# Kernel tuning notes

Hardware: AMD Instinct MI355X
Metric: run time of the kernel (lower is better)

## Reference

```python
import jax, jax.numpy as jnp
import numpy as np

B, T, F, H = 512, 512, 32, 64  # batch, lag, n_features, hidden_sizes[0]


def _lstm_layer(x_seq, Wih, Whh, bih, bhh):
    """Single LSTM layer, batch_first input [B,T,Fin] -> [B,T,H].
    PyTorch gate order: i, f, g, o."""
    # Precompute input projections for all timesteps (one big GEMM)
    xg = jnp.einsum('btf,gf->btg', x_seq, Wih) + bih + bhh  # [B,T,4H]
    xg_t = jnp.transpose(xg, (1, 0, 2))  # [T,B,4H]
    h0 = jnp.zeros((x_seq.shape[0], Whh.shape[1]), x_seq.dtype)
    c0 = jnp.zeros_like(h0)

    def step(carry, g_t):
        h, c = carry
        gates = g_t + h @ Whh.T  # [B,4H]
        i, f, g, o = jnp.split(gates, 4, axis=-1)
        i = jax.nn.sigmoid(i)
        f = jax.nn.sigmoid(f)
        g = jnp.tanh(g)
        o = jax.nn.sigmoid(o)
        c = f * c + i * g
        h = o * jnp.tanh(c)
        return (h, c), h

    (_, _), hs = jax.lax.scan(step, (h0, c0), xg_t)  # hs: [T,B,H]
    return jnp.transpose(hs, (1, 0, 2))  # [B,T,H]


def setup_inputs() -> dict:
    key = jax.random.key(0)
    ks = jax.random.split(key, 12)
    s_in = 1.0 / np.sqrt(H)
    u = lambda k, shape: jax.random.uniform(k, shape, jnp.float32, -s_in, s_in)
    return {
        'x': jax.random.normal(ks[0], (B, T, F), jnp.float32),
        'Wih0': u(ks[1], (4 * H, F)),
        'Whh0': u(ks[2], (4 * H, H)),
        'bih0': u(ks[3], (4 * H,)),
        'bhh0': u(ks[4], (4 * H,)),
        'Wih1': u(ks[5], (4 * H, H)),
        'Whh1': u(ks[6], (4 * H, H)),
        'bih1': u(ks[7], (4 * H,)),
        'bhh1': u(ks[8], (4 * H,)),
        'fcW': u(ks[9], (1, H)),
        'fcb': u(ks[10], (1,)),
    }


def reference(x, Wih0, Whh0, bih0, bhh0, Wih1, Whh1, bih1, bhh1, fcW, fcb):
    h1 = _lstm_layer(x, Wih0, Whh0, bih0, bhh0)   # [B,T,H]
    h2 = _lstm_layer(h1, Wih1, Whh1, bih1, bhh1)  # [B,T,H]  (dropout=0 at inference)
    last = h2[:, -1, :]                           # [B,H]
    out = last @ fcW.T + fcb                      # [B,1]
    return out.squeeze(-1)                        # [B]
```

## Files before the change

### kernel.cpp

```cpp
#include <hip/hip_runtime.h>
#include <math.h>

#define Bsz 512
#define Tsz 512
#define Fin 32
#define Hd 64
#define CHUNK 32
#define NCH (Tsz / CHUNK)

typedef float v2f __attribute__((ext_vector_type(2)));

__device__ __forceinline__ float fsig(float x) {
    return 1.0f / (1.0f + __expf(-x));
}
__device__ __forceinline__ float ftanh(float x) {
    float ax = fabsf(x);
    float e  = __expf(-2.0f * ax);
    float t  = (1.0f - e) / (1.0f + e);
    return copysignf(t, x);
}

__global__ __launch_bounds__(256, 2)
void lstm_layer0(const float* __restrict__ x,
                 const float4* __restrict__ Wih4,
                 const float4* __restrict__ Whh4,
                 const float* __restrict__ bih,
                 const float* __restrict__ bhh,
                 float* __restrict__ h1out)
{
    __shared__ __align__(16) float xbuf[2][CHUNK * Fin];
    __shared__ __align__(16) float hbuf[CHUNK * Hd];
    __shared__ __align__(16) float hcopy[4][Hd];
    __shared__ float glds[2][Hd * 5];

    const int tid  = threadIdx.x;
    const int lane = tid & 63;
    const int wv   = tid >> 6;
    const int b    = blockIdx.x;

    float4 wih[8];
#pragma unroll
    for (int q = 0; q < 8; ++q) wih[q] = Wih4[tid * 8 + q];
    float4 whh[16];
#pragma unroll
    for (int q = 0; q < 16; ++q) whh[q] = Whh4[tid * 16 + q];
    const float bias = bih[tid] + bhh[tid];
    const bool is_tanh_gate = (wv == 2);

    float c = 0.0f;
    hcopy[wv][lane] = 0.0f;

    const float4* xsrc = (const float4*)(x + (size_t)b * Tsz * Fin);
    ((float4*)xbuf[0])[tid] = xsrc[tid];
    __syncthreads();

    for (int ci = 0; ci < NCH; ++ci) {
        const int cur = ci & 1;
        if (ci + 1 < NCH)
            ((float4*)xbuf[cur ^ 1])[tid] = xsrc[(ci + 1) * (CHUNK * Fin / 4) + tid];
#pragma unroll 1
        for (int ct = 0; ct < CHUNK; ++ct) {
            const int t = ci * CHUNK + ct;
            const int p = t & 1;
            const float4* xrow = (const float4*)&xbuf[cur][ct * Fin];
            const float4* hrow = (const float4*)&hcopy[wv][0];

            v2f acc0 = {bias, 0.0f};
            v2f acc1 = {0.0f, 0.0f};
#pragma unroll
            for (int q = 0; q < 8; ++q) {
                float4 xv = xrow[q];
                v2f b0 = {xv.x, xv.y}, b1 = {xv.z, xv.w};
                v2f w0 = {wih[q].x, wih[q].y}, w1 = {wih[q].z, wih[q].w};
                acc0 = __builtin_elementwise_fma(b0, w0, acc0);
                acc1 = __builtin_elementwise_fma(b1, w1, acc1);
            }
#pragma unroll
            for (int q = 0; q < 16; ++q) {
                float4 hv = hrow[q];
                v2f b0 = {hv.x, hv.y}, b1 = {hv.z, hv.w};
                v2f w0 = {whh[q].x, whh[q].y}, w1 = {whh[q].z, whh[q].w};
                acc0 = __builtin_elementwise_fma(b0, w0, acc0);
                acc1 = __builtin_elementwise_fma(b1, w1, acc1);
            }
            float a = (acc0.x + acc0.y) + (acc1.x + acc1.y);
            glds[p][lane * 5 + wv] = is_tanh_gate ? ftanh(a) : fsig(a);
            __syncthreads();
            float gi = glds[p][lane * 5 + 0];
            float gf = glds[p][lane * 5 + 1];
            float gg = glds[p][lane * 5 + 2];
            float go = glds[p][lane * 5 + 3];
            c = gf * c + gi * gg;
            float h = go * ftanh(c);
            hcopy[wv][lane] = h;
            if (wv == 0) hbuf[ct * Hd + lane] = h;
        }
        __syncthreads();
        float4* dst = (float4*)(h1out + (size_t)b * Tsz * Hd + (size_t)ci * CHUNK * Hd);
        dst[tid]       = ((const float4*)hbuf)[tid];
        dst[tid + 256] = ((const float4*)hbuf)[tid + 256];
    }
}

__global__ __launch_bounds__(256, 2)
void lstm_layer1_fc(const float* __restrict__ h1,
                    const float4* __restrict__ Wih4,
                    const float4* __restrict__ Whh4,
                    const float* __restrict__ bih,
                    const float* __restrict__ bhh,
                    const float* __restrict__ fcW,
                    const float* __restrict__ fcb,
                    float* __restrict__ out)
{
    __shared__ __align__(16) float xbuf[2][CHUNK * Hd];
    __shared__ __align__(16) float hcopy[4][Hd];
    __shared__ float glds[2][Hd * 5];

    const int tid  = threadIdx.x;
    const int lane = tid & 63;
    const int wv   = tid >> 6;
    const int b    = blockIdx.x;

    float4 wih[16];
#pragma unroll
    for (int q = 0; q < 16; ++q) wih[q] = Wih4[tid * 16 + q];
    float4 whh[16];
#pragma unroll
    for (int q = 0; q < 16; ++q) whh[q] = Whh4[tid * 16 + q];
    const float bias = bih[tid] + bhh[tid];
    const bool is_tanh_gate = (wv == 2);

    float c  = 0.0f;
    float hl = 0.0f;
    hcopy[wv][lane] = 0.0f;

    const float4* xsrc = (const float4*)(h1 + (size_t)b * Tsz * Hd);
    ((float4*)xbuf[0])[tid]       = xsrc[tid];
    ((float4*)xbuf[0])[tid + 256] = xsrc[tid + 256];
    __syncthreads();

    for (int ci = 0; ci < NCH; ++ci) {
        const int cur = ci & 1;
        if (ci + 1 < NCH) {
            ((float4*)xbuf[cur ^ 1])[tid]       = xsrc[(ci + 1) * (CHUNK * Hd / 4) + tid];
            ((float4*)xbuf[cur ^ 1])[tid + 256] = xsrc[(ci + 1) * (CHUNK * Hd / 4) + tid + 256];
        }
#pragma unroll 1
        for (int ct = 0; ct < CHUNK; ++ct) {
            const int t = ci * CHUNK + ct;
            const int p = t & 1;
            const float4* xrow = (const float4*)&xbuf[cur][ct * Hd];
            const float4* hrow = (const float4*)&hcopy[wv][0];

            v2f acc0 = {bias, 0.0f};
            v2f acc1 = {0.0f, 0.0f};
#pragma unroll
            for (int q = 0; q < 16; ++q) {
                float4 xv = xrow[q];
                v2f b0 = {xv.x, xv.y}, b1 = {xv.z, xv.w};
                v2f w0 = {wih[q].x, wih[q].y}, w1 = {wih[q].z, wih[q].w};
                acc0 = __builtin_elementwise_fma(b0, w0, acc0);
                acc1 = __builtin_elementwise_fma(b1, w1, acc1);
            }
#pragma unroll
            for (int q = 0; q < 16; ++q) {
                float4 hv = hrow[q];
                v2f b0 = {hv.x, hv.y}, b1 = {hv.z, hv.w};
                v2f w0 = {whh[q].x, whh[q].y}, w1 = {whh[q].z, whh[q].w};
                acc0 = __builtin_elementwise_fma(b0, w0, acc0);
                acc1 = __builtin_elementwise_fma(b1, w1, acc1);
            }
            float a = (acc0.x + acc0.y) + (acc1.x + acc1.y);
            glds[p][lane * 5 + wv] = is_tanh_gate ? ftanh(a) : fsig(a);
            __syncthreads();
            float gi = glds[p][lane * 5 + 0];
            float gf = glds[p][lane * 5 + 1];
            float gg = glds[p][lane * 5 + 2];
            float go = glds[p][lane * 5 + 3];
            c  = gf * c + gi * gg;
            hl = go * ftanh(c);
            hcopy[wv][lane] = hl;
        }
    }
    if (wv == 0) {
        float psum = hl * fcW[lane];
#pragma unroll
        for (int off = 32; off > 0; off >>= 1)
            psum += __shfl_down(psum, off);
        if (lane == 0) out[b] = psum + fcb[0];
    }
}

extern "C" void kernel_launch(void* const* d_in, const int* in_sizes, int n_in,
                              void* d_out, int out_size, void* d_ws, size_t ws_size,
                              hipStream_t stream)
{
    const float* x    = (const float*)d_in[0];
    const float* Wih0 = (const float*)d_in[1];
    const float* Whh0 = (const float*)d_in[2];
    const float* bih0 = (const float*)d_in[3];
    const float* bhh0 = (const float*)d_in[4];
    const float* Wih1 = (const float*)d_in[5];
    const float* Whh1 = (const float*)d_in[6];
    const float* bih1 = (const float*)d_in[7];
    const float* bhh1 = (const float*)d_in[8];
    const float* fcW  = (const float*)d_in[9];
    const float* fcb  = (const float*)d_in[10];
    float* out = (float*)d_out;
    float* h1  = (float*)d_ws;

    lstm_layer0<<<dim3(Bsz), dim3(256), 0, stream>>>(
        x, (const float4*)Wih0, (const float4*)Whh0, bih0, bhh0, h1);
    lstm_layer1_fc<<<dim3(Bsz), dim3(256), 0, stream>>>(
        h1, (const float4*)Wih1, (const float4*)Whh1, bih1, bhh1, fcW, fcb, out);
}
```

Before: 850.1 us.

## Split gate dot products across thread pairs and prefetch next-step input projection

Each LSTM gate row is now computed by two threads, each covering half the reduction dimension, and the halves are combined with a lane shuffle. Blocks grow from 256 to 512 threads, which halves the serial FMA chain on the recurrent critical path. The input projection for the next timestep is computed before the per-step barrier, so only the recurrent h·Whh part stays on the dependency chain. The costs are an extra shuffle per step, more redundant cell-state updates across eight waves, and a larger block that may reduce how many blocks fit per CU.

```diff
diff --git a/kernel.cpp b/kernel.cpp
--- a/kernel.cpp
+++ b/kernel.cpp
@@ -20,7 +20,7 @@
     return copysignf(t, x);
 }
 
-__global__ __launch_bounds__(256, 2)
+__global__ __launch_bounds__(512, 4)
 void lstm_layer0(const float* __restrict__ x,
                  const float4* __restrict__ Wih4,
                  const float4* __restrict__ Whh4,
@@ -30,61 +30,72 @@
 {
     __shared__ __align__(16) float xbuf[2][CHUNK * Fin];
     __shared__ __align__(16) float hbuf[CHUNK * Hd];
-    __shared__ __align__(16) float hcopy[4][Hd];
+    __shared__ __align__(16) float hcopy[8][Hd];
     __shared__ float glds[2][Hd * 5];
 
     const int tid  = threadIdx.x;
     const int lane = tid & 63;
     const int wv   = tid >> 6;
+    const int g    = tid >> 1;
+    const int half = tid & 1;
     const int b    = blockIdx.x;
 
-    float4 wih[8];
-#pragma unroll
-    for (int q = 0; q < 8; ++q) wih[q] = Wih4[tid * 8 + q];
-    float4 whh[16];
-#pragma unroll
-    for (int q = 0; q < 16; ++q) whh[q] = Whh4[tid * 16 + q];
-    const float bias = bih[tid] + bhh[tid];
-    const bool is_tanh_gate = (wv == 2);
+    float4 wih[4];
+#pragma unroll
+    for (int q = 0; q < 4; ++q) wih[q] = Wih4[g * 8 + half * 4 + q];
+    float4 whh[8];
+#pragma unroll
+    for (int q = 0; q < 16 / 2; ++q) whh[q] = Whh4[g * 16 + half * 8 + q];
+    const float bias = half ? 0.0f : (bih[g] + bhh[g]);
+    const bool is_tanh_gate = ((g >> 6) == 2);
 
     float c = 0.0f;
     hcopy[wv][lane] = 0.0f;
 
     const float4* xsrc = (const float4*)(x + (size_t)b * Tsz * Fin);
-    ((float4*)xbuf[0])[tid] = xsrc[tid];
+    if (tid < 256) ((float4*)xbuf[0])[tid] = xsrc[tid];
     __syncthreads();
+
+    auto xdot = [&](const float* xrow_base) -> float {
+        const float4* xr = (const float4*)xrow_base + half * 4;
+        v2f a0 = {bias, 0.0f}, a1 = {0.0f, 0.0f};
+#pragma unroll
+        for (int q = 0; q < 4; ++q) {
+            float4 xv = xr[q];
+            v2f b0 = {xv.x, xv.y}, b1 = {xv.z, xv.w};
+            v2f w0 = {wih[q].x, wih[q].y}, w1 = {wih[q].z, wih[q].w};
+            a0 = __builtin_elementwise_fma(b0, w0, a0);
+            a1 = __builtin_elementwise_fma(b1, w1, a1);
+        }
+        return (a0.x + a0.y) + (a1.x + a1.y);
+    };
+
+    float ax = xdot(&xbuf[0][0]);
 
     for (int ci = 0; ci < NCH; ++ci) {
         const int cur = ci & 1;
-        if (ci + 1 < NCH)
+        if (ci + 1 < NCH && tid < 256)
             ((float4*)xbuf[cur ^ 1])[tid] = xsrc[(ci + 1) * (CHUNK * Fin / 4) + tid];
 #pragma unroll 1
         for (int ct = 0; ct < CHUNK; ++ct) {
             const int t = ci * CHUNK + ct;
             const int p = t & 1;
-            const float4* xrow = (const float4*)&xbuf[cur][ct * Fin];
-            const float4* hrow = (const float4*)&hcopy[wv][0];
-
-            v2f acc0 = {bias, 0.0f};
-            v2f acc1 = {0.0f, 0.0f};
+            const float4* hr = (const float4*)&hcopy[wv][0] + half * 8;
+            v2f a0 = {ax, 0.0f}, a1 = {0.0f, 0.0f};
 #pragma unroll
             for (int q = 0; q < 8; ++q) {
-                float4 xv = xrow[q];
-                v2f b0 = {xv.x, xv.y}, b1 = {xv.z, xv.w};
-                v2f w0 = {wih[q].x, wih[q].y}, w1 = {wih[q].z, wih[q].w};
-                acc0 = __builtin_elementwise_fma(b0, w0, acc0);
-                acc1 = __builtin_elementwise_fma(b1, w1, acc1);
-            }
-#pragma unroll
-            for (int q = 0; q < 16; ++q) {
-                float4 hv = hrow[q];
+                float4 hv = hr[q];
                 v2f b0 = {hv.x, hv.y}, b1 = {hv.z, hv.w};
                 v2f w0 = {whh[q].x, whh[q].y}, w1 = {whh[q].z, whh[q].w};
-                acc0 = __builtin_elementwise_fma(b0, w0, acc0);
-                acc1 = __builtin_elementwise_fma(b1, w1, acc1);
+                a0 = __builtin_elementwise_fma(b0, w0, a0);
+                a1 = __builtin_elementwise_fma(b1, w1, a1);
             }
-            float a = (acc0.x + acc0.y) + (acc1.x + acc1.y);
-            glds[p][lane * 5 + wv] = is_tanh_gate ? ftanh(a) : fsig(a);
+            float ah = (a0.x + a0.y) + (a1.x + a1.y);
+            float a  = ah + __shfl_xor(ah, 1);
+            float act = is_tanh_gate ? ftanh(a) : fsig(a);
+            if (!half) glds[p][(g & 63) * 5 + (g >> 6)] = act;
+            if (ct + 1 < CHUNK)      ax = xdot(&xbuf[cur][(ct + 1) * Fin]);
+            else if (ci + 1 < NCH)   ax = xdot(&xbuf[cur ^ 1][0]);
             __syncthreads();
             float gi = glds[p][lane * 5 + 0];
             float gf = glds[p][lane * 5 + 1];
@@ -97,12 +108,11 @@
         }
         __syncthreads();
         float4* dst = (float4*)(h1out + (size_t)b * Tsz * Hd + (size_t)ci * CHUNK * Hd);
-        dst[tid]       = ((const float4*)hbuf)[tid];
-        dst[tid + 256] = ((const float4*)hbuf)[tid + 256];
+        dst[tid] = ((const float4*)hbuf)[tid];
     }
 }
 
-__global__ __launch_bounds__(256, 2)
+__global__ __launch_bounds__(512, 4)
 void lstm_layer1_fc(const float* __restrict__ h1,
                     const float4* __restrict__ Wih4,
                     const float4* __restrict__ Whh4,
@@ -113,65 +123,73 @@
                     float* __restrict__ out)
 {
     __shared__ __align__(16) float xbuf[2][CHUNK * Hd];
-    __shared__ __align__(16) float hcopy[4][Hd];
+    __shared__ __align__(16) float hcopy[8][Hd];
     __shared__ float glds[2][Hd * 5];
 
     const int tid  = threadIdx.x;
     const int lane = tid & 63;
     const int wv   = tid >> 6;
+    const int g    = tid >> 1;
+    const int half = tid & 1;
     const int b    = blockIdx.x;
 
-    float4 wih[16];
-#pragma unroll
-    for (int q = 0; q < 16; ++q) wih[q] = Wih4[tid * 16 + q];
-    float4 whh[16];
-#pragma unroll
-    for (int q = 0; q < 16; ++q) whh[q] = Whh4[tid * 16 + q];
-    const float bias = bih[tid] + bhh[tid];
-    const bool is_tanh_gate = (wv == 2);
+    float4 wih[8];
+#pragma unroll
+    for (int q = 0; q < 8; ++q) wih[q] = Wih4[g * 16 + half * 8 + q];
+    float4 whh[8];
+#pragma unroll
+    for (int q = 0; q < 8; ++q) whh[q] = Whh4[g * 16 + half * 8 + q];
+    const float bias = half ? 0.0f : (bih[g] + bhh[g]);
+    const bool is_tanh_gate = ((g >> 6) == 2);
 
     float c  = 0.0f;
     float hl = 0.0f;
     hcopy[wv][lane] = 0.0f;
 
     const float4* xsrc = (const float4*)(h1 + (size_t)b * Tsz * Hd);
-    ((float4*)xbuf[0])[tid]       = xsrc[tid];
-    ((float4*)xbuf[0])[tid + 256] = xsrc[tid + 256];
+    ((float4*)xbuf[0])[tid] = xsrc[tid];
     __syncthreads();
+
+    auto xdot = [&](const float* xrow_base) -> float {
+        const float4* xr = (const float4*)xrow_base + half * 8;
+        v2f a0 = {bias, 0.0f}, a1 = {0.0f, 0.0f};
+#pragma unroll
+        for (int q = 0; q < 8; ++q) {
+            float4 xv = xr[q];
+            v2f b0 = {xv.x, xv.y}, b1 = {xv.z, xv.w};
+            v2f w0 = {wih[q].x, wih[q].y}, w1 = {wih[q].z, wih[q].w};
+            a0 = __builtin_elementwise_fma(b0, w0, a0);
+            a1 = __builtin_elementwise_fma(b1, w1, a1);
+        }
+        return (a0.x + a0.y) + (a1.x + a1.y);
+    };
+
+    float ax = xdot(&xbuf[0][0]);
 
     for (int ci = 0; ci < NCH; ++ci) {
         const int cur = ci & 1;
-        if (ci + 1 < NCH) {
-            ((float4*)xbuf[cur ^ 1])[tid]       = xsrc[(ci + 1) * (CHUNK * Hd / 4) + tid];
-            ((float4*)xbuf[cur ^ 1])[tid + 256] = xsrc[(ci + 1) * (CHUNK * Hd / 4) + tid + 256];
-        }
+        if (ci + 1 < NCH)
+            ((float4*)xbuf[cur ^ 1])[tid] = xsrc[(ci + 1) * (CHUNK * Hd / 4) + tid];
 #pragma unroll 1
         for (int ct = 0; ct < CHUNK; ++ct) {
             const int t = ci * CHUNK + ct;
             const int p = t & 1;
-            const float4* xrow = (const float4*)&xbuf[cur][ct * Hd];
-            const float4* hrow = (const float4*)&hcopy[wv][0];
-
-            v2f acc0 = {bias, 0.0f};
-            v2f acc1 = {0.0f, 0.0f};
-#pragma unroll
-            for (int q = 0; q < 16; ++q) {
-                float4 xv = xrow[q];
-                v2f b0 = {xv.x, xv.y}, b1 = {xv.z, xv.w};
-                v2f w0 = {wih[q].x, wih[q].y}, w1 = {wih[q].z, wih[q].w};
-                acc0 = __builtin_elementwise_fma(b0, w0, acc0);
-                acc1 = __builtin_elementwise_fma(b1, w1, acc1);
-            }
-#pragma unroll
-            for (int q = 0; q < 16; ++q) {
-                float4 hv = hrow[q];
+            const float4* hr = (const float4*)&hcopy[wv][0] + half * 8;
+            v2f a0 = {ax, 0.0f}, a1 = {0.0f, 0.0f};
+#pragma unroll
+            for (int q = 0; q < 8; ++q) {
+                float4 hv = hr[q];
                 v2f b0 = {hv.x, hv.y}, b1 = {hv.z, hv.w};
                 v2f w0 = {whh[q].x, whh[q].y}, w1 = {whh[q].z, whh[q].w};
-                acc0 = __builtin_elementwise_fma(b0, w0, acc0);
-                acc1 = __builtin_elementwise_fma(b1, w1, acc1);
+                a0 = __builtin_elementwise_fma(b0, w0, a0);
+                a1 = __builtin_elementwise_fma(b1, w1, a1);
             }
-            float a = (acc0.x + acc0.y) + (acc1.x + acc1.y);
-            glds[p][lane * 5 + wv] = is_tanh_gate ? ftanh(a) : fsig(a);
+            float ah = (a0.x + a0.y) + (a1.x + a1.y);
+            float a  = ah + __shfl_xor(ah, 1);
+            float act = is_tanh_gate ? ftanh(a) : fsig(a);
+            if (!half) glds[p][(g & 63) * 5 + (g >> 6)] = act;
+            if (ct + 1 < CHUNK)      ax = xdot(&xbuf[cur][(ct + 1) * Hd]);
+            else if (ci + 1 < NCH)   ax = xdot(&xbuf[cur ^ 1][0]);
             __syncthreads();
             float gi = glds[p][lane * 5 + 0];
             float gf = glds[p][lane * 5 + 1];
@@ -209,8 +227,8 @@
     float* out = (float*)d_out;
     float* h1  = (float*)d_ws;
 
-    lstm_layer0<<<dim3(Bsz), dim3(256), 0, stream>>>(
+    lstm_layer0<<<dim3(Bsz), dim3(512), 0, stream>>>(
         x, (const float4*)Wih0, (const float4*)Whh0, bih0, bhh0, h1);
-    lstm_layer1_fc<<<dim3(Bsz), dim3(256), 0, stream>>>(
+    lstm_layer1_fc<<<dim3(Bsz), dim3(512), 0, stream>>>(
         h1, (const float4*)Wih1, (const float4*)Whh1, bih1, bhh1, fcW, fcb, out);
 }
```

Result: slower. 879.2 us (+3.4%).
